# Optimization experiments

Measured on AMD Instinct MI355X. Metric: run time of the kernel, lower is better.

## Reference

```python
import jax, jax.numpy as jnp
import numpy as np

B, S, H = 8, 2048, 512

def setup_inputs() -> dict:
    key = jax.random.key(0)
    k1, k2, k3 = jax.random.split(key, 3)
    # scale inputs down so unstabilized exp(Q.x) stays finite (module has no softmax max-subtract)
    input_data = jax.random.normal(k1, (B, S, H), dtype=jnp.float32) * 0.05
    W = jax.random.normal(k2, (H, H), dtype=jnp.float32) * (1.0 / np.sqrt(H))
    b = jax.random.normal(k3, (H,), dtype=jnp.float32) * 0.01
    return {"input_data": input_data, "W": W, "b": b}

def reference(input_data, W, b):
    # Q[b,i,:] = Linear(input_data[b,i,:])  -- the 'correlated value'
    q = jnp.einsum('bsh,oh->bso', input_data, W) + b            # [B,S,H]
    # score[b,i,j] = exp( Q_i . x_j )   (no max-subtraction, faithful to original)
    scores = jnp.exp(jnp.einsum('bih,bjh->bij', q, input_data))  # [B,S,S]
    # strictly-causal mask: triu(ones,1).T == lower-triangular with zero diagonal (j < i)
    mask = jnp.tril(jnp.ones((S, S), dtype=input_data.dtype), k=-1)
    masked = scores * mask                                       # [B,S,S]
    denom = jnp.sum(masked, axis=-1, keepdims=True) + 1e-10      # [B,S,1]
    attn = masked / denom                                        # [B,S,S]
    # weighted sum of raw inputs over past positions j
    out = jnp.einsum('bij,bjh->bih', attn, input_data)           # [B,S,H]
    return out
```

## Files before the change

kernel.cpp:

```cpp
#include <hip/hip_runtime.h>
#include <hip/hip_bf16.h>

#define BATCH 8
#define SEQ   2048
#define DIM   512

typedef __bf16 bf16x8 __attribute__((ext_vector_type(8)));
typedef float  f32x4  __attribute__((ext_vector_type(4)));

__device__ __forceinline__ ushort f2bf(float f) {
    union { float f; unsigned u; } c; c.f = f;
    unsigned u = c.u;
    u += 0x7fffu + ((u >> 16) & 1u);
    return (ushort)(u >> 16);
}

__global__ __launch_bounds__(256) void prep_kernel(const float* __restrict__ X,
                                                   ushort* __restrict__ Xb,
                                                   ushort* __restrict__ Xt) {
    __shared__ ushort T[32 * 33];
    int t   = threadIdx.x;
    int bid = blockIdx.x;
    int b   = bid >> 10;
    int st  = (bid >> 4) & 63;
    int ht  = bid & 15;
    int s0 = st * 32, h0 = ht * 32;

    int r  = t >> 3;
    int c4 = (t & 7) * 4;
    size_t src = ((size_t)(b * SEQ + s0 + r)) * DIM + h0 + c4;
    float4 v = *(const float4*)(X + src);
    ushort u0 = f2bf(v.x), u1 = f2bf(v.y), u2 = f2bf(v.z), u3 = f2bf(v.w);
    ushort4 uv; uv.x = u0; uv.y = u1; uv.z = u2; uv.w = u3;
    *(ushort4*)(Xb + src) = uv;
    T[(c4 + 0) * 33 + r] = u0;
    T[(c4 + 1) * 33 + r] = u1;
    T[(c4 + 2) * 33 + r] = u2;
    T[(c4 + 3) * 33 + r] = u3;
    __syncthreads();
    int hh = t >> 3;
    int sc = (t & 7) * 4;
    ushort4 w;
    w.x = T[hh * 33 + sc + 0];
    w.y = T[hh * 33 + sc + 1];
    w.z = T[hh * 33 + sc + 2];
    w.w = T[hh * 33 + sc + 3];
    *(ushort4*)(Xt + ((size_t)(b * DIM + h0 + hh)) * SEQ + s0 + sc) = w;
}

__global__ __launch_bounds__(256) void wconv_kernel(const float* __restrict__ W,
                                                    ushort* __restrict__ Wb) {
    int gt = blockIdx.x * 256 + threadIdx.x;
    size_t base = (size_t)gt * 8;
    float4 a = *(const float4*)(W + base);
    float4 c = *(const float4*)(W + base + 4);
    ushort4 lo, hi;
    lo.x = f2bf(a.x); lo.y = f2bf(a.y); lo.z = f2bf(a.z); lo.w = f2bf(a.w);
    hi.x = f2bf(c.x); hi.y = f2bf(c.y); hi.z = f2bf(c.z); hi.w = f2bf(c.w);
    *(ushort4*)(Wb + base)     = lo;
    *(ushort4*)(Wb + base + 4) = hi;
}

#define GEMM_COMPUTE(CUR)                                                                  \
    {                                                                                      \
        bf16x8 af[4], bfr[4];                                                              \
        _Pragma("unroll") for (int r = 0; r < 4; ++r)                                      \
            af[r] = *(const bf16x8*)&At[CUR][(wr * 64 + r * 16 + ln) * 40 + lg * 8];       \
        _Pragma("unroll") for (int cc = 0; cc < 4; ++cc)                                   \
            bfr[cc] = *(const bf16x8*)&Bt[CUR][(wc * 64 + cc * 16 + ln) * 40 + lg * 8];    \
        _Pragma("unroll") for (int r = 0; r < 4; ++r)                                      \
            _Pragma("unroll") for (int cc = 0; cc < 4; ++cc)                               \
                acc[r][cc] = __builtin_amdgcn_mfma_f32_16x16x32_bf16(af[r], bfr[cc],       \
                                                                     acc[r][cc], 0, 0, 0); \
    }

#define GEMM_STORE(CUR, A0, A1, B0, B1)                   \
    {                                                     \
        *(uint4*)&At[CUR][srow * 40 + sc8]        = A0;   \
        *(uint4*)&At[CUR][(64 + srow) * 40 + sc8] = A1;   \
        *(uint4*)&Bt[CUR][srow * 40 + sc8]        = B0;   \
        *(uint4*)&Bt[CUR][(64 + srow) * 40 + sc8] = B1;   \
    }

__global__ __launch_bounds__(256, 2) void qgemm_kernel(const ushort* __restrict__ Xb,
                                                       const ushort* __restrict__ Wb,
                                                       const float* __restrict__ bias,
                                                       ushort* __restrict__ Qb) {
    __shared__ ushort At[2][128 * 40];
    __shared__ ushort Bt[2][128 * 40];
    int t   = threadIdx.x;
    int bid = blockIdx.x;
    int mt = bid >> 2, nt = bid & 3;
    int m0 = mt << 7, n0 = nt << 7;
    int w  = t >> 6, l = t & 63, ln = l & 15, lg = l >> 4;
    int wr = w >> 1, wc = w & 1;

    f32x4 acc[4][4] = {};
    int srow = t >> 2;
    int sc8  = (t & 3) * 8;

    const ushort* Arow = Xb + (size_t)m0 * 512;
    const ushort* Brow = Wb + (size_t)n0 * 512;

#define QG_LOAD(KS, A0, A1, B0, B1)                                                \
    A0 = *(const uint4*)(Arow + (size_t)srow * 512 + (KS) * 32 + sc8);             \
    A1 = *(const uint4*)(Arow + (size_t)(64 + srow) * 512 + (KS) * 32 + sc8);      \
    B0 = *(const uint4*)(Brow + (size_t)srow * 512 + (KS) * 32 + sc8);             \
    B1 = *(const uint4*)(Brow + (size_t)(64 + srow) * 512 + (KS) * 32 + sc8);

    uint4 pA0, pA1, pB0, pB1, qA0, qA1, qB0, qB1;
    QG_LOAD(0, pA0, pA1, pB0, pB1)
    QG_LOAD(1, qA0, qA1, qB0, qB1)
    GEMM_STORE(0, pA0, pA1, pB0, pB1)
    __syncthreads();
    for (int ks = 0; ks < 14; ks += 2) {
        QG_LOAD(ks + 2, pA0, pA1, pB0, pB1)
        GEMM_COMPUTE(0)
        GEMM_STORE(1, qA0, qA1, qB0, qB1)
        __syncthreads();
        QG_LOAD(ks + 3, qA0, qA1, qB0, qB1)
        GEMM_COMPUTE(1)
        GEMM_STORE(0, pA0, pA1, pB0, pB1)
        __syncthreads();
    }
    GEMM_COMPUTE(0)
    GEMM_STORE(1, qA0, qA1, qB0, qB1)
    __syncthreads();
    GEMM_COMPUTE(1)

    float bv[4];
#pragma unroll
    for (int c = 0; c < 4; ++c) bv[c] = bias[n0 + wc * 64 + c * 16 + ln];
#pragma unroll
    for (int r = 0; r < 4; ++r)
#pragma unroll
        for (int c = 0; c < 4; ++c)
#pragma unroll
            for (int q = 0; q < 4; ++q) {
                int row = m0 + wr * 64 + r * 16 + lg * 4 + q;
                int col = n0 + wc * 64 + c * 16 + ln;
                Qb[(size_t)row * 512 + col] = f2bf(acc[r][c][q] + bv[c]);
            }
}

__global__ __launch_bounds__(256, 2) void sgemm_kernel(const ushort* __restrict__ Qb,
                                                       const ushort* __restrict__ Xb,
                                                       ushort* __restrict__ Pb,
                                                       float* __restrict__ den,
                                                       int g0, int G) {
    __shared__ ushort At[2][128 * 40];
    __shared__ ushort Bt[2][128 * 40];
    int t  = threadIdx.x;
    int bL = blockIdx.x;
    int b  = g0 + bL;
    int c  = blockIdx.y;
    int it = 0, base = 0;
    for (;;) { if (c < base + it + 1) break; base += it + 1; ++it; }
    int jt = c - base;

    int m0 = it << 7, n0 = jt << 7;
    int w  = t >> 6, l = t & 63, ln = l & 15, lg = l >> 4;
    int wr = w >> 1, wc = w & 1;

    const ushort* Arow = Qb + (size_t)(b * SEQ + m0) * 512;
    const ushort* Brow = Xb + (size_t)(b * SEQ + n0) * 512;

    f32x4 acc[4][4] = {};
    int srow = t >> 2;
    int sc8  = (t & 3) * 8;

#define SG_LOAD(KS, A0, A1, B0, B1)                                                \
    A0 = *(const uint4*)(Arow + (size_t)srow * 512 + (KS) * 32 + sc8);             \
    A1 = *(const uint4*)(Arow + (size_t)(64 + srow) * 512 + (KS) * 32 + sc8);      \
    B0 = *(const uint4*)(Brow + (size_t)srow * 512 + (KS) * 32 + sc8);             \
    B1 = *(const uint4*)(Brow + (size_t)(64 + srow) * 512 + (KS) * 32 + sc8);

    uint4 pA0, pA1, pB0, pB1, qA0, qA1, qB0, qB1;
    SG_LOAD(0, pA0, pA1, pB0, pB1)
    SG_LOAD(1, qA0, qA1, qB0, qB1)
    GEMM_STORE(0, pA0, pA1, pB0, pB1)
    __syncthreads();
    for (int ks = 0; ks < 14; ks += 2) {
        SG_LOAD(ks + 2, pA0, pA1, pB0, pB1)
        GEMM_COMPUTE(0)
        GEMM_STORE(1, qA0, qA1, qB0, qB1)
        __syncthreads();
        SG_LOAD(ks + 3, qA0, qA1, qB0, qB1)
        GEMM_COMPUTE(1)
        GEMM_STORE(0, pA0, pA1, pB0, pB1)
        __syncthreads();
    }
    GEMM_COMPUTE(0)
    GEMM_STORE(1, qA0, qA1, qB0, qB1)
    __syncthreads();
    GEMM_COMPUTE(1)

    ushort* ptile = Pb + ((size_t)c * G + bL) * 16384;
#pragma unroll
    for (int r = 0; r < 4; ++r)
#pragma unroll
        for (int q = 0; q < 4; ++q) {
            int row  = wr * 64 + r * 16 + lg * 4 + q;
            int grow = m0 + row;
            float rs = 0.f;
#pragma unroll
            for (int cc = 0; cc < 4; ++cc) {
                int col = n0 + wc * 64 + cc * 16 + ln;
                float ex = (col < grow) ? __expf(acc[r][cc][q]) : 0.f;
                rs += ex;
                ptile[row * 128 + (wc * 64 + cc * 16 + ln)] = f2bf(ex);
            }
            rs += __shfl_xor(rs, 1);
            rs += __shfl_xor(rs, 2);
            rs += __shfl_xor(rs, 4);
            rs += __shfl_xor(rs, 8);
            if (ln == 0) unsafeAtomicAdd(&den[b * SEQ + grow], rs);
        }
}

__global__ __launch_bounds__(256, 2) void pvgemm_kernel(const ushort* __restrict__ Pb,
                                                        const ushort* __restrict__ Xt,
                                                        const float* __restrict__ den,
                                                        float* __restrict__ out,
                                                        int g0, int G) {
    __shared__ ushort At[2][128 * 40];
    __shared__ ushort Bt2[2][64 * 40];
    int t  = threadIdx.x;
    int bL = blockIdx.x;
    int b  = g0 + bL;
    int y  = blockIdx.y;
    int p  = y >> 3;
    int ht = y & 7;
    int n0 = ht << 6;

    int w = t >> 6, l = t & 63, ln = l & 15, lg = l >> 4;
    int wr = w >> 1, wc = w & 1;
    int srow = t >> 2;
    int sc8  = (t & 3) * 8;

    const ushort* BrowX = Xt + ((size_t)b * DIM + n0) * SEQ;

#define PV_LOAD(KK, A0, A1, B0)                                                    \
    {                                                                              \
        const ushort* ptile = Pb + ((size_t)(Tit + ((KK) >> 2)) * G + bL) * 16384  \
                              + ((KK) & 3) * 32;                                   \
        A0 = *(const uint4*)(ptile + srow * 128 + sc8);                            \
        A1 = *(const uint4*)(ptile + (64 + srow) * 128 + sc8);                     \
        B0 = *(const uint4*)(BrowX + (size_t)srow * SEQ + (KK) * 32 + sc8);        \
    }
#define PV_ST(CUR, A0, A1, B0)                              \
    {                                                       \
        *(uint4*)&At[CUR][srow * 40 + sc8]        = A0;     \
        *(uint4*)&At[CUR][(64 + srow) * 40 + sc8] = A1;     \
        *(uint4*)&Bt2[CUR][srow * 40 + sc8]       = B0;     \
    }
#define PV_COMPUTE(CUR)                                                                   \
    {                                                                                     \
        bf16x8 af[4], bfr[2];                                                             \
        _Pragma("unroll") for (int r = 0; r < 4; ++r)                                     \
            af[r] = *(const bf16x8*)&At[CUR][(wr * 64 + r * 16 + ln) * 40 + lg * 8];      \
        _Pragma("unroll") for (int cc = 0; cc < 2; ++cc)                                  \
            bfr[cc] = *(const bf16x8*)&Bt2[CUR][(wc * 32 + cc * 16 + ln) * 40 + lg * 8];  \
        _Pragma("unroll") for (int r = 0; r < 4; ++r)                                     \
            _Pragma("unroll") for (int cc = 0; cc < 2; ++cc)                              \
                acc[r][cc] = __builtin_amdgcn_mfma_f32_16x16x32_bf16(af[r], bfr[cc],      \
                                                                     acc[r][cc], 0, 0, 0);\
    }

    for (int half = 0; half < 2; ++half) {
        int it  = half ? p : (15 - p);
        int Tit = (it * (it + 1)) >> 1;
        int n   = (it + 1) * 4;
        int m0  = it << 7;
        f32x4 acc[4][2] = {};

        uint4 pA0, pA1, pB0, qA0, qA1, qB0;
        PV_LOAD(0, pA0, pA1, pB0)
        PV_LOAD(1, qA0, qA1, qB0)
        __syncthreads();
        PV_ST(0, pA0, pA1, pB0)
        __syncthreads();
        for (int ks = 0; ks < n - 2; ks += 2) {
            PV_LOAD(ks + 2, pA0, pA1, pB0)
            PV_COMPUTE(0)
            PV_ST(1, qA0, qA1, qB0)
            __syncthreads();
            if (ks + 3 < n) PV_LOAD(ks + 3, qA0, qA1, qB0)
            PV_COMPUTE(1)
            PV_ST(0, pA0, pA1, pB0)
            __syncthreads();
        }
        PV_COMPUTE(0)
        PV_ST(1, qA0, qA1, qB0)
        __syncthreads();
        PV_COMPUTE(1)

#pragma unroll
        for (int r = 0; r < 4; ++r)
#pragma unroll
            for (int q = 0; q < 4; ++q) {
                int row = m0 + wr * 64 + r * 16 + lg * 4 + q;
                float inv = 1.0f / (den[b * SEQ + row] + 1e-10f);
                size_t o = (size_t)(b * SEQ + row) * 512;
#pragma unroll
                for (int cc = 0; cc < 2; ++cc)
                    out[o + n0 + wc * 32 + cc * 16 + ln] = acc[r][cc][q] * inv;
            }
    }
}

extern "C" void kernel_launch(void* const* d_in, const int* in_sizes, int n_in,
                              void* d_out, int out_size, void* d_ws, size_t ws_size,
                              hipStream_t stream) {
    const float* X    = (const float*)d_in[0];
    const float* W    = (const float*)d_in[1];
    const float* bias = (const float*)d_in[2];
    float* out = (float*)d_out;

    ushort* ws = (ushort*)d_ws;
    ushort* Xb = ws;
    ushort* Xt = ws + 8388608;
    ushort* Qb = ws + 16777216;
    ushort* Wb = ws + 25165824;
    float*  den = (float*)((char*)d_ws + 50855936);
    ushort* Pb = (ushort*)((char*)d_ws + 50921472);

    size_t avail = (ws_size > 50921472) ? (ws_size - 50921472) : 0;
    int G = 1;
    while (G < 8 && (size_t)(G * 2) * 4456448 <= avail) G *= 2;

    hipMemsetAsync(den, 0, (size_t)BATCH * SEQ * sizeof(float), stream);
    prep_kernel<<<dim3(8192), dim3(256), 0, stream>>>(X, Xb, Xt);
    wconv_kernel<<<dim3(128), dim3(256), 0, stream>>>(W, Wb);
    qgemm_kernel<<<dim3(512), dim3(256), 0, stream>>>(Xb, Wb, bias, Qb);
    for (int g0 = 0; g0 < BATCH; g0 += G) {
        sgemm_kernel<<<dim3(G, 136), dim3(256), 0, stream>>>(Qb, Xb, Pb, den, g0, G);
        pvgemm_kernel<<<dim3(G, 64), dim3(256), 0, stream>>>(Pb, Xt, den, out, g0, G);
    }
}
```

Measured before the change: 109.9 us.

## Use 256x128 tiles with 512-thread blocks for Q and score GEMMs, fuse weight conversion

After: 127.3 us. +15.8%, slower.

```diff
diff --git a/kernel.cpp b/kernel.cpp
--- a/kernel.cpp
+++ b/kernel.cpp
@@ -17,10 +17,24 @@
 
 __global__ __launch_bounds__(256) void prep_kernel(const float* __restrict__ X,
                                                    ushort* __restrict__ Xb,
-                                                   ushort* __restrict__ Xt) {
+                                                   ushort* __restrict__ Xt,
+                                                   const float* __restrict__ W,
+                                                   ushort* __restrict__ Wb) {
     __shared__ ushort T[32 * 33];
     int t   = threadIdx.x;
     int bid = blockIdx.x;
+    if (bid >= 8192) {
+        int gt = (bid - 8192) * 256 + t;
+        size_t base = (size_t)gt * 8;
+        float4 a = *(const float4*)(W + base);
+        float4 c = *(const float4*)(W + base + 4);
+        ushort4 lo, hi;
+        lo.x = f2bf(a.x); lo.y = f2bf(a.y); lo.z = f2bf(a.z); lo.w = f2bf(a.w);
+        hi.x = f2bf(c.x); hi.y = f2bf(c.y); hi.z = f2bf(c.z); hi.w = f2bf(c.w);
+        *(ushort4*)(Wb + base)     = lo;
+        *(ushort4*)(Wb + base + 4) = hi;
+        return;
+    }
     int b   = bid >> 10;
     int st  = (bid >> 4) & 63;
     int ht  = bid & 15;
@@ -48,173 +62,148 @@
     *(ushort4*)(Xt + ((size_t)(b * DIM + h0 + hh)) * SEQ + s0 + sc) = w;
 }
 
-__global__ __launch_bounds__(256) void wconv_kernel(const float* __restrict__ W,
-                                                    ushort* __restrict__ Wb) {
-    int gt = blockIdx.x * 256 + threadIdx.x;
-    size_t base = (size_t)gt * 8;
-    float4 a = *(const float4*)(W + base);
-    float4 c = *(const float4*)(W + base + 4);
-    ushort4 lo, hi;
-    lo.x = f2bf(a.x); lo.y = f2bf(a.y); lo.z = f2bf(a.z); lo.w = f2bf(a.w);
-    hi.x = f2bf(c.x); hi.y = f2bf(c.y); hi.z = f2bf(c.z); hi.w = f2bf(c.w);
-    *(ushort4*)(Wb + base)     = lo;
-    *(ushort4*)(Wb + base + 4) = hi;
-}
-
-#define GEMM_COMPUTE(CUR)                                                                  \
+#define C256_COMPUTE(CUR)                                                                  \
     {                                                                                      \
         bf16x8 af[4], bfr[4];                                                              \
         _Pragma("unroll") for (int r = 0; r < 4; ++r)                                      \
-            af[r] = *(const bf16x8*)&At[CUR][(wr * 64 + r * 16 + ln) * 40 + lg * 8];       \
+            af[r] = *(const bf16x8*)&At[CUR][(wrow * 64 + r * 16 + ln) * 40 + lg * 8];     \
         _Pragma("unroll") for (int cc = 0; cc < 4; ++cc)                                   \
-            bfr[cc] = *(const bf16x8*)&Bt[CUR][(wc * 64 + cc * 16 + ln) * 40 + lg * 8];    \
+            bfr[cc] = *(const bf16x8*)&Bt[CUR][(wcol * 64 + cc * 16 + ln) * 40 + lg * 8];  \
         _Pragma("unroll") for (int r = 0; r < 4; ++r)                                      \
             _Pragma("unroll") for (int cc = 0; cc < 4; ++cc)                               \
                 acc[r][cc] = __builtin_amdgcn_mfma_f32_16x16x32_bf16(af[r], bfr[cc],       \
                                                                      acc[r][cc], 0, 0, 0); \
     }
 
-#define GEMM_STORE(CUR, A0, A1, B0, B1)                   \
-    {                                                     \
-        *(uint4*)&At[CUR][srow * 40 + sc8]        = A0;   \
-        *(uint4*)&At[CUR][(64 + srow) * 40 + sc8] = A1;   \
-        *(uint4*)&Bt[CUR][srow * 40 + sc8]        = B0;   \
-        *(uint4*)&Bt[CUR][(64 + srow) * 40 + sc8] = B1;   \
-    }
-
-__global__ __launch_bounds__(256, 2) void qgemm_kernel(const ushort* __restrict__ Xb,
+#define C256_LOAD(KS)                                                                  \
+    {                                                                                  \
+        const ushort* pa_ = Arow + (size_t)arow * 512 + (KS) * 32 + acol;              \
+        a0 = *(const uint4*)pa_;                                                       \
+        a1 = *(const uint4*)(pa_ + 8);                                                 \
+        b0 = *(const uint4*)(Brow + (size_t)brow * 512 + (KS) * 32 + bcol);            \
+    }
+#define C256_STORE(CUR)                                                                \
+    {                                                                                  \
+        *(uint4*)&At[CUR][arow * 40 + acol]     = a0;                                  \
+        *(uint4*)&At[CUR][arow * 40 + acol + 8] = a1;                                  \
+        *(uint4*)&Bt[CUR][brow * 40 + bcol]     = b0;                                  \
+    }
+
+__global__ __launch_bounds__(512, 4) void qgemm_kernel(const ushort* __restrict__ Xb,
                                                        const ushort* __restrict__ Wb,
                                                        const float* __restrict__ bias,
                                                        ushort* __restrict__ Qb) {
-    __shared__ ushort At[2][128 * 40];
+    __shared__ ushort At[2][256 * 40];
     __shared__ ushort Bt[2][128 * 40];
     int t   = threadIdx.x;
     int bid = blockIdx.x;
     int mt = bid >> 2, nt = bid & 3;
-    int m0 = mt << 7, n0 = nt << 7;
+    int m0 = mt << 8, n0 = nt << 7;
     int w  = t >> 6, l = t & 63, ln = l & 15, lg = l >> 4;
-    int wr = w >> 1, wc = w & 1;
+    int wrow = w >> 1, wcol = w & 1;
 
     f32x4 acc[4][4] = {};
-    int srow = t >> 2;
-    int sc8  = (t & 3) * 8;
-
     const ushort* Arow = Xb + (size_t)m0 * 512;
     const ushort* Brow = Wb + (size_t)n0 * 512;
-
-#define QG_LOAD(KS, A0, A1, B0, B1)                                                \
-    A0 = *(const uint4*)(Arow + (size_t)srow * 512 + (KS) * 32 + sc8);             \
-    A1 = *(const uint4*)(Arow + (size_t)(64 + srow) * 512 + (KS) * 32 + sc8);      \
-    B0 = *(const uint4*)(Brow + (size_t)srow * 512 + (KS) * 32 + sc8);             \
-    B1 = *(const uint4*)(Brow + (size_t)(64 + srow) * 512 + (KS) * 32 + sc8);
-
-    uint4 pA0, pA1, pB0, pB1, qA0, qA1, qB0, qB1;
-    QG_LOAD(0, pA0, pA1, pB0, pB1)
-    QG_LOAD(1, qA0, qA1, qB0, qB1)
-    GEMM_STORE(0, pA0, pA1, pB0, pB1)
+    int arow = t >> 1, acol = (t & 1) * 16;
+    int brow = t >> 2, bcol = (t & 3) * 8;
+
+    uint4 a0, a1, b0;
+    C256_LOAD(0)
+    C256_STORE(0)
     __syncthreads();
-    for (int ks = 0; ks < 14; ks += 2) {
-        QG_LOAD(ks + 2, pA0, pA1, pB0, pB1)
-        GEMM_COMPUTE(0)
-        GEMM_STORE(1, qA0, qA1, qB0, qB1)
-        __syncthreads();
-        QG_LOAD(ks + 3, qA0, qA1, qB0, qB1)
-        GEMM_COMPUTE(1)
-        GEMM_STORE(0, pA0, pA1, pB0, pB1)
-        __syncthreads();
-    }
-    GEMM_COMPUTE(0)
-    GEMM_STORE(1, qA0, qA1, qB0, qB1)
-    __syncthreads();
-    GEMM_COMPUTE(1)
+    int cur = 0;
+    for (int ks = 0; ks < 16; ++ks) {
+        if (ks < 15) C256_LOAD(ks + 1)
+        C256_COMPUTE(cur)
+        if (ks < 15) C256_STORE(cur ^ 1)
+        __syncthreads();
+        cur ^= 1;
+    }
 
     float bv[4];
 #pragma unroll
-    for (int c = 0; c < 4; ++c) bv[c] = bias[n0 + wc * 64 + c * 16 + ln];
+    for (int c = 0; c < 4; ++c) bv[c] = bias[n0 + wcol * 64 + c * 16 + ln];
 #pragma unroll
     for (int r = 0; r < 4; ++r)
 #pragma unroll
         for (int c = 0; c < 4; ++c)
 #pragma unroll
             for (int q = 0; q < 4; ++q) {
-                int row = m0 + wr * 64 + r * 16 + lg * 4 + q;
-                int col = n0 + wc * 64 + c * 16 + ln;
+                int row = m0 + wrow * 64 + r * 16 + lg * 4 + q;
+                int col = n0 + wcol * 64 + c * 16 + ln;
                 Qb[(size_t)row * 512 + col] = f2bf(acc[r][c][q] + bv[c]);
             }
 }
 
-__global__ __launch_bounds__(256, 2) void sgemm_kernel(const ushort* __restrict__ Qb,
+__global__ __launch_bounds__(512, 4) void sgemm_kernel(const ushort* __restrict__ Qb,
                                                        const ushort* __restrict__ Xb,
                                                        ushort* __restrict__ Pb,
                                                        float* __restrict__ den,
                                                        int g0, int G) {
-    __shared__ ushort At[2][128 * 40];
+    __shared__ ushort At[2][256 * 40];
     __shared__ ushort Bt[2][128 * 40];
     int t  = threadIdx.x;
-    int bL = blockIdx.x;
+    int bL = blockIdx.y;
     int b  = g0 + bL;
-    int c  = blockIdx.y;
-    int it = 0, base = 0;
-    for (;;) { if (c < base + it + 1) break; base += it + 1; ++it; }
-    int jt = c - base;
-
-    int m0 = it << 7, n0 = jt << 7;
+    int c  = blockIdx.x;
+    int rt = 7, rem = c;
+    for (;;) { int n = 2 * rt + 2; if (rem < n) break; rem -= n; --rt; }
+    int jt = rem;
+
+    int m0 = rt << 8, n0 = jt << 7;
     int w  = t >> 6, l = t & 63, ln = l & 15, lg = l >> 4;
-    int wr = w >> 1, wc = w & 1;
+    int wrow = w >> 1, wcol = w & 1;
 
     const ushort* Arow = Qb + (size_t)(b * SEQ + m0) * 512;
     const ushort* Brow = Xb + (size_t)(b * SEQ + n0) * 512;
 
     f32x4 acc[4][4] = {};
-    int srow = t >> 2;
-    int sc8  = (t & 3) * 8;
-
-#define SG_LOAD(KS, A0, A1, B0, B1)                                                \
-    A0 = *(const uint4*)(Arow + (size_t)srow * 512 + (KS) * 32 + sc8);             \
-    A1 = *(const uint4*)(Arow + (size_t)(64 + srow) * 512 + (KS) * 32 + sc8);      \
-    B0 = *(const uint4*)(Brow + (size_t)srow * 512 + (KS) * 32 + sc8);             \
-    B1 = *(const uint4*)(Brow + (size_t)(64 + srow) * 512 + (KS) * 32 + sc8);
-
-    uint4 pA0, pA1, pB0, pB1, qA0, qA1, qB0, qB1;
-    SG_LOAD(0, pA0, pA1, pB0, pB1)
-    SG_LOAD(1, qA0, qA1, qB0, qB1)
-    GEMM_STORE(0, pA0, pA1, pB0, pB1)
+    int arow = t >> 1, acol = (t & 1) * 16;
+    int brow = t >> 2, bcol = (t & 3) * 8;
+
+    uint4 a0, a1, b0;
+    C256_LOAD(0)
+    C256_STORE(0)
     __syncthreads();
-    for (int ks = 0; ks < 14; ks += 2) {
-        SG_LOAD(ks + 2, pA0, pA1, pB0, pB1)
-        GEMM_COMPUTE(0)
-        GEMM_STORE(1, qA0, qA1, qB0, qB1)
-        __syncthreads();
-        SG_LOAD(ks + 3, qA0, qA1, qB0, qB1)
-        GEMM_COMPUTE(1)
-        GEMM_STORE(0, pA0, pA1, pB0, pB1)
-        __syncthreads();
-    }
-    GEMM_COMPUTE(0)
-    GEMM_STORE(1, qA0, qA1, qB0, qB1)
-    __syncthreads();
-    GEMM_COMPUTE(1)
-
-    ushort* ptile = Pb + ((size_t)c * G + bL) * 16384;
+    int cur = 0;
+    for (int ks = 0; ks < 16; ++ks) {
+        if (ks < 15) C256_LOAD(ks + 1)
+        C256_COMPUTE(cur)
+        if (ks < 15) C256_STORE(cur ^ 1)
+        __syncthreads();
+        cur ^= 1;
+    }
+
+    int it   = 2 * rt + (wrow >> 1);
+    bool ok  = (wrow >= 2) || (jt <= 2 * rt);
+    int Tidx = ((it * (it + 1)) >> 1) + jt;
+    ushort* ptile = Pb + ((size_t)Tidx * G + bL) * 16384;
 #pragma unroll
     for (int r = 0; r < 4; ++r)
 #pragma unroll
         for (int q = 0; q < 4; ++q) {
-            int row  = wr * 64 + r * 16 + lg * 4 + q;
-            int grow = m0 + row;
+            int lrow = wrow * 64 + r * 16 + lg * 4 + q;
+            int grow = m0 + lrow;
             float rs = 0.f;
+            float ex[4];
 #pragma unroll
             for (int cc = 0; cc < 4; ++cc) {
-                int col = n0 + wc * 64 + cc * 16 + ln;
-                float ex = (col < grow) ? __expf(acc[r][cc][q]) : 0.f;
-                rs += ex;
-                ptile[row * 128 + (wc * 64 + cc * 16 + ln)] = f2bf(ex);
+                int col = n0 + wcol * 64 + cc * 16 + ln;
+                ex[cc] = (col < grow) ? __expf(acc[r][cc][q]) : 0.f;
+                rs += ex[cc];
+            }
+            if (ok) {
+                int prow = lrow & 127;
+#pragma unroll
+                for (int cc = 0; cc < 4; ++cc)
+                    ptile[prow * 128 + (wcol * 64 + cc * 16 + ln)] = f2bf(ex[cc]);
             }
             rs += __shfl_xor(rs, 1);
             rs += __shfl_xor(rs, 2);
             rs += __shfl_xor(rs, 4);
             rs += __shfl_xor(rs, 8);
-            if (ln == 0) unsafeAtomicAdd(&den[b * SEQ + grow], rs);
+            if (ok && ln == 0) unsafeAtomicAdd(&den[b * SEQ + grow], rs);
         }
 }
 
@@ -223,8 +212,8 @@
                                                         const float* __restrict__ den,
                                                         float* __restrict__ out,
                                                         int g0, int G) {
-    __shared__ ushort At[2][128 * 40];
-    __shared__ ushort Bt2[2][64 * 40];
+    __shared__ ushort Ap[2][128 * 40];
+    __shared__ ushort Bp[2][64 * 40];
     int t  = threadIdx.x;
     int bL = blockIdx.x;
     int b  = g0 + bL;
@@ -250,17 +239,17 @@
     }
 #define PV_ST(CUR, A0, A1, B0)                              \
     {                                                       \
-        *(uint4*)&At[CUR][srow * 40 + sc8]        = A0;     \
-        *(uint4*)&At[CUR][(64 + srow) * 40 + sc8] = A1;     \
-        *(uint4*)&Bt2[CUR][srow * 40 + sc8]       = B0;     \
+        *(uint4*)&Ap[CUR][srow * 40 + sc8]        = A0;     \
+        *(uint4*)&Ap[CUR][(64 + srow) * 40 + sc8] = A1;     \
+        *(uint4*)&Bp[CUR][srow * 40 + sc8]        = B0;     \
     }
 #define PV_COMPUTE(CUR)                                                                   \
     {                                                                                     \
         bf16x8 af[4], bfr[2];                                                             \
         _Pragma("unroll") for (int r = 0; r < 4; ++r)                                     \
-            af[r] = *(const bf16x8*)&At[CUR][(wr * 64 + r * 16 + ln) * 40 + lg * 8];      \
+            af[r] = *(const bf16x8*)&Ap[CUR][(wr * 64 + r * 16 + ln) * 40 + lg * 8];      \
         _Pragma("unroll") for (int cc = 0; cc < 2; ++cc)                                  \
-            bfr[cc] = *(const bf16x8*)&Bt2[CUR][(wc * 32 + cc * 16 + ln) * 40 + lg * 8];  \
+            bfr[cc] = *(const bf16x8*)&Bp[CUR][(wc * 32 + cc * 16 + ln) * 40 + lg * 8];   \
         _Pragma("unroll") for (int r = 0; r < 4; ++r)                                     \
             _Pragma("unroll") for (int cc = 0; cc < 2; ++cc)                              \
                 acc[r][cc] = __builtin_amdgcn_mfma_f32_16x16x32_bf16(af[r], bfr[cc],      \
@@ -306,6 +295,7 @@
                 for (int cc = 0; cc < 2; ++cc)
                     out[o + n0 + wc * 32 + cc * 16 + ln] = acc[r][cc][q] * inv;
             }
+        __syncthreads();
     }
 }
 
@@ -330,11 +320,10 @@
     while (G < 8 && (size_t)(G * 2) * 4456448 <= avail) G *= 2;
 
     hipMemsetAsync(den, 0, (size_t)BATCH * SEQ * sizeof(float), stream);
-    prep_kernel<<<dim3(8192), dim3(256), 0, stream>>>(X, Xb, Xt);
-    wconv_kernel<<<dim3(128), dim3(256), 0, stream>>>(W, Wb);
-    qgemm_kernel<<<dim3(512), dim3(256), 0, stream>>>(Xb, Wb, bias, Qb);
+    prep_kernel<<<dim3(8320), dim3(256), 0, stream>>>(X, Xb, Xt, W, Wb);
+    qgemm_kernel<<<dim3(256), dim3(512), 0, stream>>>(Xb, Wb, bias, Qb);
     for (int g0 = 0; g0 < BATCH; g0 += G) {
-        sgemm_kernel<<<dim3(G, 136), dim3(256), 0, stream>>>(Qb, Xb, Pb, den, g0, G);
+        sgemm_kernel<<<dim3(72, G), dim3(512), 0, stream>>>(Qb, Xb, Pb, den, g0, G);
         pvgemm_kernel<<<dim3(G, 64), dim3(256), 0, stream>>>(Pb, Xt, den, out, g0, G);
     }
 }
```

## Compute softmax denominators in PV gemm, drop atomics and memset, merge weight conversion

Applied to the files above, without the earlier changes.

Measured after the change: 118.0 us. +7.4%, slower.

```diff
diff --git a/kernel.cpp b/kernel.cpp
--- a/kernel.cpp
+++ b/kernel.cpp
@@ -17,10 +17,24 @@
 
 __global__ __launch_bounds__(256) void prep_kernel(const float* __restrict__ X,
                                                    ushort* __restrict__ Xb,
-                                                   ushort* __restrict__ Xt) {
+                                                   ushort* __restrict__ Xt,
+                                                   const float* __restrict__ W,
+                                                   ushort* __restrict__ Wb) {
     __shared__ ushort T[32 * 33];
     int t   = threadIdx.x;
     int bid = blockIdx.x;
+    if (bid >= 8192) {
+        int gt = (bid - 8192) * 256 + t;
+        size_t base = (size_t)gt * 8;
+        float4 a = *(const float4*)(W + base);
+        float4 c = *(const float4*)(W + base + 4);
+        ushort4 lo, hi;
+        lo.x = f2bf(a.x); lo.y = f2bf(a.y); lo.z = f2bf(a.z); lo.w = f2bf(a.w);
+        hi.x = f2bf(c.x); hi.y = f2bf(c.y); hi.z = f2bf(c.z); hi.w = f2bf(c.w);
+        *(ushort4*)(Wb + base)     = lo;
+        *(ushort4*)(Wb + base + 4) = hi;
+        return;
+    }
     int b   = bid >> 10;
     int st  = (bid >> 4) & 63;
     int ht  = bid & 15;
@@ -48,41 +62,7 @@
     *(ushort4*)(Xt + ((size_t)(b * DIM + h0 + hh)) * SEQ + s0 + sc) = w;
 }
 
-__global__ __launch_bounds__(256) void wconv_kernel(const float* __restrict__ W,
-                                                    ushort* __restrict__ Wb) {
-    int gt = blockIdx.x * 256 + threadIdx.x;
-    size_t base = (size_t)gt * 8;
-    float4 a = *(const float4*)(W + base);
-    float4 c = *(const float4*)(W + base + 4);
-    ushort4 lo, hi;
-    lo.x = f2bf(a.x); lo.y = f2bf(a.y); lo.z = f2bf(a.z); lo.w = f2bf(a.w);
-    hi.x = f2bf(c.x); hi.y = f2bf(c.y); hi.z = f2bf(c.z); hi.w = f2bf(c.w);
-    *(ushort4*)(Wb + base)     = lo;
-    *(ushort4*)(Wb + base + 4) = hi;
-}
-
-#define GEMM_COMPUTE(CUR)                                                                  \
-    {                                                                                      \
-        bf16x8 af[4], bfr[4];                                                              \
-        _Pragma("unroll") for (int r = 0; r < 4; ++r)                                      \
-            af[r] = *(const bf16x8*)&At[CUR][(wr * 64 + r * 16 + ln) * 40 + lg * 8];       \
-        _Pragma("unroll") for (int cc = 0; cc < 4; ++cc)                                   \
-            bfr[cc] = *(const bf16x8*)&Bt[CUR][(wc * 64 + cc * 16 + ln) * 40 + lg * 8];    \
-        _Pragma("unroll") for (int r = 0; r < 4; ++r)                                      \
-            _Pragma("unroll") for (int cc = 0; cc < 4; ++cc)                               \
-                acc[r][cc] = __builtin_amdgcn_mfma_f32_16x16x32_bf16(af[r], bfr[cc],       \
-                                                                     acc[r][cc], 0, 0, 0); \
-    }
-
-#define GEMM_STORE(CUR, A0, A1, B0, B1)                   \
-    {                                                     \
-        *(uint4*)&At[CUR][srow * 40 + sc8]        = A0;   \
-        *(uint4*)&At[CUR][(64 + srow) * 40 + sc8] = A1;   \
-        *(uint4*)&Bt[CUR][srow * 40 + sc8]        = B0;   \
-        *(uint4*)&Bt[CUR][(64 + srow) * 40 + sc8] = B1;   \
-    }
-
-__global__ __launch_bounds__(256, 2) void qgemm_kernel(const ushort* __restrict__ Xb,
+__global__ __launch_bounds__(256, 3) void qgemm_kernel(const ushort* __restrict__ Xb,
                                                        const ushort* __restrict__ Wb,
                                                        const float* __restrict__ bias,
                                                        ushort* __restrict__ Qb) {
@@ -108,25 +88,46 @@
     B0 = *(const uint4*)(Brow + (size_t)srow * 512 + (KS) * 32 + sc8);             \
     B1 = *(const uint4*)(Brow + (size_t)(64 + srow) * 512 + (KS) * 32 + sc8);
 
+#define QG_STORE(CUR, A0, A1, B0, B1)                     \
+    {                                                     \
+        *(uint4*)&At[CUR][srow * 40 + sc8]        = A0;   \
+        *(uint4*)&At[CUR][(64 + srow) * 40 + sc8] = A1;   \
+        *(uint4*)&Bt[CUR][srow * 40 + sc8]        = B0;   \
+        *(uint4*)&Bt[CUR][(64 + srow) * 40 + sc8] = B1;   \
+    }
+
+#define QG_COMPUTE(CUR)                                                                    \
+    {                                                                                      \
+        bf16x8 af[4], bfr[4];                                                              \
+        _Pragma("unroll") for (int r = 0; r < 4; ++r)                                      \
+            af[r] = *(const bf16x8*)&At[CUR][(wr * 64 + r * 16 + ln) * 40 + lg * 8];       \
+        _Pragma("unroll") for (int cc = 0; cc < 4; ++cc)                                   \
+            bfr[cc] = *(const bf16x8*)&Bt[CUR][(wc * 64 + cc * 16 + ln) * 40 + lg * 8];    \
+        _Pragma("unroll") for (int r = 0; r < 4; ++r)                                      \
+            _Pragma("unroll") for (int cc = 0; cc < 4; ++cc)                               \
+                acc[r][cc] = __builtin_amdgcn_mfma_f32_16x16x32_bf16(af[r], bfr[cc],       \
+                                                                     acc[r][cc], 0, 0, 0); \
+    }
+
     uint4 pA0, pA1, pB0, pB1, qA0, qA1, qB0, qB1;
     QG_LOAD(0, pA0, pA1, pB0, pB1)
     QG_LOAD(1, qA0, qA1, qB0, qB1)
-    GEMM_STORE(0, pA0, pA1, pB0, pB1)
+    QG_STORE(0, pA0, pA1, pB0, pB1)
     __syncthreads();
     for (int ks = 0; ks < 14; ks += 2) {
         QG_LOAD(ks + 2, pA0, pA1, pB0, pB1)
-        GEMM_COMPUTE(0)
-        GEMM_STORE(1, qA0, qA1, qB0, qB1)
+        QG_COMPUTE(0)
+        QG_STORE(1, qA0, qA1, qB0, qB1)
         __syncthreads();
         QG_LOAD(ks + 3, qA0, qA1, qB0, qB1)
-        GEMM_COMPUTE(1)
-        GEMM_STORE(0, pA0, pA1, pB0, pB1)
-        __syncthreads();
-    }
-    GEMM_COMPUTE(0)
-    GEMM_STORE(1, qA0, qA1, qB0, qB1)
-    __syncthreads();
-    GEMM_COMPUTE(1)
+        QG_COMPUTE(1)
+        QG_STORE(0, pA0, pA1, pB0, pB1)
+        __syncthreads();
+    }
+    QG_COMPUTE(0)
+    QG_STORE(1, qA0, qA1, qB0, qB1)
+    __syncthreads();
+    QG_COMPUTE(1)
 
     float bv[4];
 #pragma unroll
@@ -143,13 +144,13 @@
             }
 }
 
-__global__ __launch_bounds__(256, 2) void sgemm_kernel(const ushort* __restrict__ Qb,
+__global__ __launch_bounds__(256, 3) void sgemm_kernel(const ushort* __restrict__ Qb,
                                                        const ushort* __restrict__ Xb,
                                                        ushort* __restrict__ Pb,
-                                                       float* __restrict__ den,
                                                        int g0, int G) {
-    __shared__ ushort At[2][128 * 40];
-    __shared__ ushort Bt[2][128 * 40];
+    __shared__ ushort SMEM[20480];
+#define SG_AT(C) (SMEM + (C) * 5120)
+#define SG_BT(C) (SMEM + 10240 + (C) * 5120)
     int t  = threadIdx.x;
     int bL = blockIdx.x;
     int b  = g0 + bL;
@@ -175,56 +176,77 @@
     B0 = *(const uint4*)(Brow + (size_t)srow * 512 + (KS) * 32 + sc8);             \
     B1 = *(const uint4*)(Brow + (size_t)(64 + srow) * 512 + (KS) * 32 + sc8);
 
+#define SG_STORE(CUR, A0, A1, B0, B1)                       \
+    {                                                       \
+        *(uint4*)&SG_AT(CUR)[srow * 40 + sc8]        = A0;  \
+        *(uint4*)&SG_AT(CUR)[(64 + srow) * 40 + sc8] = A1;  \
+        *(uint4*)&SG_BT(CUR)[srow * 40 + sc8]        = B0;  \
+        *(uint4*)&SG_BT(CUR)[(64 + srow) * 40 + sc8] = B1;  \
+    }
+
+#define SG_COMPUTE(CUR)                                                                    \
+    {                                                                                      \
+        bf16x8 af[4], bfr[4];                                                              \
+        _Pragma("unroll") for (int r = 0; r < 4; ++r)                                      \
+            af[r] = *(const bf16x8*)&SG_AT(CUR)[(wr * 64 + r * 16 + ln) * 40 + lg * 8];    \
+        _Pragma("unroll") for (int cc = 0; cc < 4; ++cc)                                   \
+            bfr[cc] = *(const bf16x8*)&SG_BT(CUR)[(wc * 64 + cc * 16 + ln) * 40 + lg * 8]; \
+        _Pragma("unroll") for (int r = 0; r < 4; ++r)                                      \
+            _Pragma("unroll") for (int cc = 0; cc < 4; ++cc)                               \
+                acc[r][cc] = __builtin_amdgcn_mfma_f32_16x16x32_bf16(af[r], bfr[cc],       \
+                                                                     acc[r][cc], 0, 0, 0); \
+    }
+
     uint4 pA0, pA1, pB0, pB1, qA0, qA1, qB0, qB1;
     SG_LOAD(0, pA0, pA1, pB0, pB1)
     SG_LOAD(1, qA0, qA1, qB0, qB1)
-    GEMM_STORE(0, pA0, pA1, pB0, pB1)
+    SG_STORE(0, pA0, pA1, pB0, pB1)
     __syncthreads();
     for (int ks = 0; ks < 14; ks += 2) {
         SG_LOAD(ks + 2, pA0, pA1, pB0, pB1)
-        GEMM_COMPUTE(0)
-        GEMM_STORE(1, qA0, qA1, qB0, qB1)
+        SG_COMPUTE(0)
+        SG_STORE(1, qA0, qA1, qB0, qB1)
         __syncthreads();
         SG_LOAD(ks + 3, qA0, qA1, qB0, qB1)
-        GEMM_COMPUTE(1)
-        GEMM_STORE(0, pA0, pA1, pB0, pB1)
-        __syncthreads();
-    }
-    GEMM_COMPUTE(0)
-    GEMM_STORE(1, qA0, qA1, qB0, qB1)
-    __syncthreads();
-    GEMM_COMPUTE(1)
+        SG_COMPUTE(1)
+        SG_STORE(0, pA0, pA1, pB0, pB1)
+        __syncthreads();
+    }
+    SG_COMPUTE(0)
+    SG_STORE(1, qA0, qA1, qB0, qB1)
+    __syncthreads();
+    SG_COMPUTE(1)
+    __syncthreads();
+
+#pragma unroll
+    for (int r = 0; r < 4; ++r)
+#pragma unroll
+        for (int q = 0; q < 4; ++q) {
+            int prow = wr * 64 + r * 16 + lg * 4 + q;
+            int grow = m0 + prow;
+#pragma unroll
+            for (int cc = 0; cc < 4; ++cc) {
+                int pcol = wc * 64 + cc * 16 + ln;
+                int col  = n0 + pcol;
+                float ex = (col < grow) ? __expf(acc[r][cc][q]) : 0.f;
+                SMEM[prow * 128 + pcol] = f2bf(ex);
+            }
+        }
+    __syncthreads();
 
     ushort* ptile = Pb + ((size_t)c * G + bL) * 16384;
 #pragma unroll
-    for (int r = 0; r < 4; ++r)
-#pragma unroll
-        for (int q = 0; q < 4; ++q) {
-            int row  = wr * 64 + r * 16 + lg * 4 + q;
-            int grow = m0 + row;
-            float rs = 0.f;
-#pragma unroll
-            for (int cc = 0; cc < 4; ++cc) {
-                int col = n0 + wc * 64 + cc * 16 + ln;
-                float ex = (col < grow) ? __expf(acc[r][cc][q]) : 0.f;
-                rs += ex;
-                ptile[row * 128 + (wc * 64 + cc * 16 + ln)] = f2bf(ex);
-            }
-            rs += __shfl_xor(rs, 1);
-            rs += __shfl_xor(rs, 2);
-            rs += __shfl_xor(rs, 4);
-            rs += __shfl_xor(rs, 8);
-            if (ln == 0) unsafeAtomicAdd(&den[b * SEQ + grow], rs);
-        }
-}
-
-__global__ __launch_bounds__(256, 2) void pvgemm_kernel(const ushort* __restrict__ Pb,
+    for (int k2 = 0; k2 < 8; ++k2)
+        *(uint4*)(ptile + k2 * 2048 + t * 8) = *(const uint4*)(SMEM + k2 * 2048 + t * 8);
+}
+
+__global__ __launch_bounds__(256, 4) void pvgemm_kernel(const ushort* __restrict__ Pb,
                                                         const ushort* __restrict__ Xt,
-                                                        const float* __restrict__ den,
                                                         float* __restrict__ out,
                                                         int g0, int G) {
-    __shared__ ushort At[2][128 * 40];
-    __shared__ ushort Bt2[2][64 * 40];
+    __shared__ ushort Ap[2][128 * 40];
+    __shared__ ushort Bp[2][64 * 40];
+    __shared__ float  dden[128];
     int t  = threadIdx.x;
     int bL = blockIdx.x;
     int b  = g0 + bL;
@@ -250,17 +272,22 @@
     }
 #define PV_ST(CUR, A0, A1, B0)                              \
     {                                                       \
-        *(uint4*)&At[CUR][srow * 40 + sc8]        = A0;     \
-        *(uint4*)&At[CUR][(64 + srow) * 40 + sc8] = A1;     \
-        *(uint4*)&Bt2[CUR][srow * 40 + sc8]       = B0;     \
+        *(uint4*)&Ap[CUR][srow * 40 + sc8]        = A0;     \
+        *(uint4*)&Ap[CUR][(64 + srow) * 40 + sc8] = A1;     \
+        *(uint4*)&Bp[CUR][srow * 40 + sc8]        = B0;     \
     }
 #define PV_COMPUTE(CUR)                                                                   \
     {                                                                                     \
         bf16x8 af[4], bfr[2];                                                             \
         _Pragma("unroll") for (int r = 0; r < 4; ++r)                                     \
-            af[r] = *(const bf16x8*)&At[CUR][(wr * 64 + r * 16 + ln) * 40 + lg * 8];      \
+            af[r] = *(const bf16x8*)&Ap[CUR][(wr * 64 + r * 16 + ln) * 40 + lg * 8];      \
         _Pragma("unroll") for (int cc = 0; cc < 2; ++cc)                                  \
-            bfr[cc] = *(const bf16x8*)&Bt2[CUR][(wc * 32 + cc * 16 + ln) * 40 + lg * 8];  \
+            bfr[cc] = *(const bf16x8*)&Bp[CUR][(wc * 32 + cc * 16 + ln) * 40 + lg * 8];   \
+        if (wc == 0) {                                                                    \
+            _Pragma("unroll") for (int r = 0; r < 4; ++r)                                 \
+                _Pragma("unroll") for (int e = 0; e < 8; ++e)                             \
+                    dsum[r] += (float)af[r][e];                                           \
+        }                                                                                 \
         _Pragma("unroll") for (int r = 0; r < 4; ++r)                                     \
             _Pragma("unroll") for (int cc = 0; cc < 2; ++cc)                              \
                 acc[r][cc] = __builtin_amdgcn_mfma_f32_16x16x32_bf16(af[r], bfr[cc],      \
@@ -273,6 +300,7 @@
         int n   = (it + 1) * 4;
         int m0  = it << 7;
         f32x4 acc[4][2] = {};
+        float dsum[4] = {0.f, 0.f, 0.f, 0.f};
 
         uint4 pA0, pA1, pB0, qA0, qA1, qB0;
         PV_LOAD(0, pA0, pA1, pB0)
@@ -295,17 +323,30 @@
         __syncthreads();
         PV_COMPUTE(1)
 
+        if (wc == 0) {
+#pragma unroll
+            for (int r = 0; r < 4; ++r) {
+                float s = dsum[r];
+                s += __shfl_xor(s, 16);
+                s += __shfl_xor(s, 32);
+                if (lg == 0) dden[wr * 64 + r * 16 + ln] = s;
+            }
+        }
+        __syncthreads();
+
 #pragma unroll
         for (int r = 0; r < 4; ++r)
 #pragma unroll
             for (int q = 0; q < 4; ++q) {
-                int row = m0 + wr * 64 + r * 16 + lg * 4 + q;
-                float inv = 1.0f / (den[b * SEQ + row] + 1e-10f);
+                int lrow = wr * 64 + r * 16 + lg * 4 + q;
+                int row  = m0 + lrow;
+                float inv = 1.0f / (dden[lrow] + 1e-10f);
                 size_t o = (size_t)(b * SEQ + row) * 512;
 #pragma unroll
                 for (int cc = 0; cc < 2; ++cc)
                     out[o + n0 + wc * 32 + cc * 16 + ln] = acc[r][cc][q] * inv;
             }
+        __syncthreads();
     }
 }
 
@@ -322,19 +363,16 @@
     ushort* Xt = ws + 8388608;
     ushort* Qb = ws + 16777216;
     ushort* Wb = ws + 25165824;
-    float*  den = (float*)((char*)d_ws + 50855936);
-    ushort* Pb = (ushort*)((char*)d_ws + 50921472);
-
-    size_t avail = (ws_size > 50921472) ? (ws_size - 50921472) : 0;
+    ushort* Pb = (ushort*)((char*)d_ws + 50855936);
+
+    size_t avail = (ws_size > 50855936) ? (ws_size - 50855936) : 0;
     int G = 1;
     while (G < 8 && (size_t)(G * 2) * 4456448 <= avail) G *= 2;
 
-    hipMemsetAsync(den, 0, (size_t)BATCH * SEQ * sizeof(float), stream);
-    prep_kernel<<<dim3(8192), dim3(256), 0, stream>>>(X, Xb, Xt);
-    wconv_kernel<<<dim3(128), dim3(256), 0, stream>>>(W, Wb);
+    prep_kernel<<<dim3(8320), dim3(256), 0, stream>>>(X, Xb, Xt, W, Wb);
     qgemm_kernel<<<dim3(512), dim3(256), 0, stream>>>(Xb, Wb, bias, Qb);
     for (int g0 = 0; g0 < BATCH; g0 += G) {
-        sgemm_kernel<<<dim3(G, 136), dim3(256), 0, stream>>>(Qb, Xb, Pb, den, g0, G);
-        pvgemm_kernel<<<dim3(G, 64), dim3(256), 0, stream>>>(Pb, Xt, den, out, g0, G);
-    }
-}
+        sgemm_kernel<<<dim3(G, 136), dim3(256), 0, stream>>>(Qb, Xb, Pb, g0, G);
+        pvgemm_kernel<<<dim3(G, 64), dim3(256), 0, stream>>>(Pb, Xt, out, g0, G);
+    }
+}
```
